# Kernel tuning notes

Hardware: AMD Instinct MI355X
Metric: run time of the kernel (lower is better)

## Reference

```python
import jax, jax.numpy as jnp
import numpy as np

B, N, D = 4, 4096, 256


def setup_inputs() -> dict:
    key = jax.random.key(0)
    k1, k2 = jax.random.split(key)
    val = jax.random.normal(k1, (B, N, D), dtype=jnp.float32)
    state = jax.random.normal(k2, (B, N), dtype=jnp.float32)
    return {"val": val, "state": state}


def reference(val, state):
    # pairwise_fn: scaled dot-product -> scores [B, N, N]
    scale = val.shape[-1] ** -0.5
    scores = jnp.einsum("bid,bjd->bij", val, val) * scale
    # edge_compress_fn = softsign (non-softmax compression)
    edges = scores / (1.0 + jnp.abs(scores))
    # state_weight_edges=False, val/state projections are Identity
    delta_state = jnp.einsum("bij,bj->bi", edges, state)   # [B, N]
    delta_val = jnp.einsum("bij,bjd->bid", edges, val)      # [B, N, D]
    return (delta_state, delta_val)
```

## Files before the change

kernel.cpp:

```cpp
#include <hip/hip_runtime.h>


#define B_  4
#define N_  4096
#define D_  256

typedef __attribute__((ext_vector_type(8))) short short8;
typedef __attribute__((ext_vector_type(4))) float floatx4;

__device__ __forceinline__ unsigned short f2bf(float f) {
    unsigned int u = __float_as_uint(f);
    u += 0x7fff + ((u >> 16) & 1);
    return (unsigned short)(u >> 16);
}

__device__ __forceinline__ void gl_lds16(const void* g, void* l) {
    __builtin_amdgcn_global_load_lds(
        (const __attribute__((address_space(1))) unsigned int*)g,
        (__attribute__((address_space(3))) unsigned int*)l, 16, 0, 0);
}
__device__ __forceinline__ void gl_lds4(const void* g, void* l) {
    __builtin_amdgcn_global_load_lds(
        (const __attribute__((address_space(1))) unsigned int*)g,
        (__attribute__((address_space(3))) unsigned int*)l, 4, 0, 0);
}

__global__ __launch_bounds__(256)
void prepass_kernel(const float* __restrict__ val,
                    unsigned short* __restrict__ Vb,
                    unsigned short* __restrict__ VF) {
    __shared__ unsigned short tile[64][68];
    const int t   = threadIdx.x;
    const int blk = blockIdx.x;
    const int b   = blk >> 8;
    const int it  = (blk >> 2) & 63;
    const int dt  = blk & 3;
    const int i0  = it * 64, d0 = dt * 64;
    const float*    vb  = val + (size_t)b * N_ * D_;
    unsigned short* Vbb = Vb  + (size_t)b * N_ * D_;
    unsigned short* VFb = VF  + (size_t)b * N_ * D_;

    #pragma unroll
    for (int q = 0; q < 4; ++q) {
        int idx = t + 256 * q;
        int row = idx >> 4;
        int c4  = idx & 15;
        float4 v = *(const float4*)(vb + (size_t)(i0 + row) * D_ + d0 + c4 * 4);
        ushort4 h;
        h.x = f2bf(v.x); h.y = f2bf(v.y); h.z = f2bf(v.z); h.w = f2bf(v.w);
        *(ushort4*)(Vbb + (size_t)(i0 + row) * D_ + d0 + c4 * 4) = h;
        *(ushort4*)&tile[row][c4 * 4] = h;
    }
    __syncthreads();
    #pragma unroll
    for (int q = 0; q < 4; ++q) {
        int dr = (t >> 4) + q * 16;
        int i4 = t & 15;
        ushort4 h;
        h.x = tile[i4 * 4 + 0][dr];
        h.y = tile[i4 * 4 + 1][dr];
        h.z = tile[i4 * 4 + 2][dr];
        h.w = tile[i4 * 4 + 3][dr];
        const int jb = (i0 >> 5) + (i4 >> 3);
        const int e  = (i4 & 7) * 4;
        *(ushort4*)(VFb + ((size_t)jb * 256 + d0 + dr) * 32 + e) = h;
    }
}

__global__ __launch_bounds__(256, 2)
void prop_main(const float* __restrict__ state,
               const unsigned short* __restrict__ Vb,
               const unsigned short* __restrict__ VF,
               float* __restrict__ dvp,
               float* __restrict__ dsp_o)
{
    __shared__ __attribute__((aligned(16))) unsigned char smem[75776];

    const int t    = threadIdx.x;
    const int w    = t >> 6;
    const int lane = t & 63;
    const int quad = lane >> 4;
    const int l16  = lane & 15;

    const int x   = blockIdx.x;
    const int it  = x >> 3;
    const int b   = (x >> 1) & 3;
    const int jh  = x & 1;
    const int it0 = it * 64;
    const int jbase = jh * 2048;
    const int niter = 32;

    unsigned short* EshL = (unsigned short*)(smem + 65536);
    float*          dsred = (float*)(smem + 75264);

    const unsigned short* Vbb = Vb + (size_t)b * N_ * D_;
    const unsigned short* VFb = VF + (size_t)b * N_ * D_;
    const float*          stb = state + (size_t)b * N_;

    const int hi  = lane >> 5;
    const int p32 = lane & 31;

    int vgoff[8];
    #pragma unroll
    for (int n = 0; n < 8; ++n) {
        int r  = 2 * (w * 8 + n) + hi;
        int gr = p32 ^ (r & 7);
        vgoff[n] = r * 256 + gr * 8;
    }

    const int r0 = (w >> 1) * 32;
    const int c0 = (w & 1) * 32;
    const int pA = l16 & 7;

    const unsigned short* vf_lane = VFb + (size_t)jh * (64 * 8192)
                                  + w * 2048 + l16 * 32 + quad * 8;

    short8 A0[8], A1[8];
    {
        const unsigned short* ar0 = Vbb + (size_t)(it0 + r0 + l16) * 256 + quad * 8;
        const unsigned short* ar1 = ar0 + 16 * 256;
        #pragma unroll
        for (int ks = 0; ks < 8; ++ks) {
            A0[ks] = *(const short8*)(ar0 + ks * 32);
            A1[ks] = *(const short8*)(ar1 + ks * 32);
        }
    }

    #pragma unroll
    for (int n = 0; n < 8; ++n)
        gl_lds16(Vbb + (size_t)jbase * 256 + vgoff[n],
                 smem + (w * 8 + n) * 1024);
    if (w == 0) gl_lds4(stb + jbase + lane, smem + 74752);

    floatx4 dv[4][4];
    #pragma unroll
    for (int a = 0; a < 4; ++a)
        #pragma unroll
        for (int c = 0; c < 4; ++c)
            dv[a][c] = (floatx4){0.f, 0.f, 0.f, 0.f};
    float dsp[8];
    #pragma unroll
    for (int k = 0; k < 8; ++k) dsp[k] = 0.f;

    for (int k = 0; k < niter; ++k) {
        const int buf = k & 1;
        unsigned short* vjL = (unsigned short*)(smem + buf * 32768);
        const float*    stj = (const float*)(smem + 74752 + buf * 256);

        __syncthreads();

        if (k + 1 < niter) {
            const size_t j0n = jbase + (size_t)(k + 1) * 64;
            #pragma unroll
            for (int n = 0; n < 8; ++n)
                gl_lds16(Vbb + j0n * 256 + vgoff[n],
                         smem + (buf ^ 1) * 32768 + (w * 8 + n) * 1024);
            if (w == 0) gl_lds4(stb + j0n + lane, smem + 74752 + (buf ^ 1) * 256);
        }

        short8 bfr[2][4];
        {
            const unsigned short* vfk = vf_lane + (size_t)k * 16384;
            #pragma unroll
            for (int ks = 0; ks < 2; ++ks)
                #pragma unroll
                for (int c2 = 0; c2 < 4; ++c2)
                    bfr[ks][c2] = *(const short8*)(vfk + ks * 8192 + c2 * 512);
        }

        floatx4 sa[2][2];
        #pragma unroll
        for (int a = 0; a < 2; ++a)
            #pragma unroll
            for (int c = 0; c < 2; ++c)
                sa[a][c] = (floatx4){0.f, 0.f, 0.f, 0.f};

        #pragma unroll
        for (int ks = 0; ks < 8; ++ks) {
            const int p = ((ks * 4 + quad) ^ pA) * 8;
            short8 b0 = *(const short8*)&vjL[(c0 + l16) * 256 + p];
            short8 b1 = *(const short8*)&vjL[(c0 + 16 + l16) * 256 + p];
            sa[0][0] = __builtin_amdgcn_mfma_f32_16x16x32_bf16(A0[ks], b0, sa[0][0], 0, 0, 0);
            sa[0][1] = __builtin_amdgcn_mfma_f32_16x16x32_bf16(A0[ks], b1, sa[0][1], 0, 0, 0);
            sa[1][0] = __builtin_amdgcn_mfma_f32_16x16x32_bf16(A1[ks], b0, sa[1][0], 0, 0, 0);
            sa[1][1] = __builtin_amdgcn_mfma_f32_16x16x32_bf16(A1[ks], b1, sa[1][1], 0, 0, 0);
        }

        float stc0 = stj[c0 + l16];
        float stc1 = stj[c0 + 16 + l16];
        #pragma unroll
        for (int a = 0; a < 2; ++a) {
            #pragma unroll
            for (int r = 0; r < 4; ++r) {
                const int il = r0 + a * 16 + quad * 4 + r;
                float s0 = sa[a][0][r];
                float s1 = sa[a][1][r];
                float e0 = s0 * __builtin_amdgcn_rcpf(16.0f + fabsf(s0));
                float e1 = s1 * __builtin_amdgcn_rcpf(16.0f + fabsf(s1));
                dsp[a * 4 + r] += e0 * stc0 + e1 * stc1;
                EshL[il * 72 + c0 + l16]      = f2bf(e0);
                EshL[il * 72 + c0 + 16 + l16] = f2bf(e1);
            }
        }
        __syncthreads();

        #pragma unroll
        for (int ks = 0; ks < 2; ++ks) {
            short8 af[4];
            #pragma unroll
            for (int a2 = 0; a2 < 4; ++a2)
                af[a2] = *(const short8*)&EshL[(a2 * 16 + l16) * 72 + ks * 32 + quad * 8];
            #pragma unroll
            for (int a2 = 0; a2 < 4; ++a2)
                #pragma unroll
                for (int c2 = 0; c2 < 4; ++c2)
                    dv[a2][c2] = __builtin_amdgcn_mfma_f32_16x16x32_bf16(af[a2], bfr[ks][c2], dv[a2][c2], 0, 0, 0);
        }
    }

    float* dvo = dvp + (size_t)jh * B_ * N_ * D_ + (size_t)b * N_ * D_
                     + (size_t)it0 * D_;
    #pragma unroll
    for (int a2 = 0; a2 < 4; ++a2)
        #pragma unroll
        for (int c2 = 0; c2 < 4; ++c2)
            #pragma unroll
            for (int r = 0; r < 4; ++r) {
                const int il = a2 * 16 + quad * 4 + r;
                const int d  = w * 64 + c2 * 16 + l16;
                dvo[(size_t)il * D_ + d] = dv[a2][c2][r];
            }

    #pragma unroll
    for (int k = 0; k < 8; ++k) {
        float v = dsp[k];
        v += __shfl_xor(v, 1);
        v += __shfl_xor(v, 2);
        v += __shfl_xor(v, 4);
        v += __shfl_xor(v, 8);
        dsp[k] = v;
    }
    if (l16 == 0) {
        #pragma unroll
        for (int a = 0; a < 2; ++a)
            #pragma unroll
            for (int r = 0; r < 4; ++r) {
                const int row = r0 + a * 16 + quad * 4 + r;
                dsred[(w & 1) * 64 + row] = dsp[a * 4 + r];
            }
    }
    __syncthreads();
    if (t < 64)
        dsp_o[(size_t)jh * B_ * N_ + (size_t)b * N_ + it0 + t]
            = dsred[t] + dsred[64 + t];
}

__global__ __launch_bounds__(256)
void combine_kernel(const float4* __restrict__ dv0, const float4* __restrict__ dv1,
                    const float*  __restrict__ ds0, const float*  __restrict__ ds1,
                    float* __restrict__ out) {
    const int NDV4 = B_ * N_ * D_ / 4;
    const int NDS  = B_ * N_;
    int x = blockIdx.x * 256 + threadIdx.x;
    if (x < NDV4) {
        float4 a = dv0[x], c = dv1[x];
        float4 r;
        r.x = a.x + c.x; r.y = a.y + c.y; r.z = a.z + c.z; r.w = a.w + c.w;
        ((float4*)(out + NDS))[x] = r;
    } else {
        int y = (x - NDV4) * 4;
        if (y < NDS) {
            float4 a = *(const float4*)(ds0 + y);
            float4 c = *(const float4*)(ds1 + y);
            float4 r;
            r.x = a.x + c.x; r.y = a.y + c.y; r.z = a.z + c.z; r.w = a.w + c.w;
            *(float4*)(out + y) = r;
        }
    }
}

__global__ __launch_bounds__(256, 1)
void prop_kernel_fb(const float* __restrict__ val,
                    const float* __restrict__ state,
                    float* __restrict__ out) {
    __shared__ __attribute__((aligned(16))) unsigned short vi[64][264];
    __shared__ __attribute__((aligned(16))) unsigned short vj[64][264];
    __shared__ __attribute__((aligned(16))) unsigned short vjt[2048][8];
    __shared__ __attribute__((aligned(16))) unsigned short Esh[64][72];
    __shared__ float stj[64];
    __shared__ float dsred[2][64];

    const int t    = threadIdx.x;
    const int w    = t >> 6;
    const int lane = t & 63;
    const int quad = lane >> 4;
    const int l16  = lane & 15;
    const int b   = blockIdx.x >> 6;
    const int it0 = (blockIdx.x & 63) << 6;
    const float* valb = val   + (size_t)b * N_ * D_;
    const float* stb  = state + (size_t)b * N_;

    #pragma unroll
    for (int n = 0; n < 16; ++n) {
        int idx = t + 256 * n;
        int row = idx >> 6;
        int c4  = idx & 63;
        float4 v = *(const float4*)(valb + (size_t)(it0 + row) * D_ + c4 * 4);
        ushort4 h;
        h.x = f2bf(v.x); h.y = f2bf(v.y); h.z = f2bf(v.z); h.w = f2bf(v.w);
        *(ushort4*)&vi[row][c4 * 4] = h;
    }

    const int r0 = (w >> 1) * 32;
    const int c0 = (w & 1) * 32;
    floatx4 dv[4][4];
    #pragma unroll
    for (int a = 0; a < 4; ++a)
        #pragma unroll
        for (int c = 0; c < 4; ++c)
            dv[a][c] = (floatx4){0.f, 0.f, 0.f, 0.f};
    float dsp[8];
    #pragma unroll
    for (int k = 0; k < 8; ++k) dsp[k] = 0.f;

    for (int jt = 0; jt < 64; ++jt) {
        const int j0 = jt * 64;
        #pragma unroll
        for (int n = 0; n < 16; ++n) {
            int idx = t + 256 * n;
            int row = idx >> 6;
            int c4  = idx & 63;
            float4 v = *(const float4*)(valb + (size_t)(j0 + row) * D_ + c4 * 4);
            ushort4 h;
            h.x = f2bf(v.x); h.y = f2bf(v.y); h.z = f2bf(v.z); h.w = f2bf(v.w);
            *(ushort4*)&vj[row][c4 * 4] = h;
        }
        if (t < 64) stj[t] = stb[j0 + t];
        __syncthreads();

        #pragma unroll
        for (int n = 0; n < 8; ++n) {
            const int d  = t;
            const int jb = n;
            short8 pk;
            #pragma unroll
            for (int jj = 0; jj < 8; ++jj) pk[jj] = (short)vj[jb * 8 + jj][d];
            *(short8*)&vjt[d * 8 + (jb ^ (d & 7))][0] = pk;
        }

        floatx4 sa[2][2];
        #pragma unroll
        for (int a = 0; a < 2; ++a)
            #pragma unroll
            for (int c = 0; c < 2; ++c)
                sa[a][c] = (floatx4){0.f, 0.f, 0.f, 0.f};
        #pragma unroll
        for (int ks = 0; ks < 8; ++ks) {
            const int d0 = ks * 32 + quad * 8;
            short8 a0 = *(const short8*)&vi[r0 + l16][d0];
            short8 a1 = *(const short8*)&vi[r0 + 16 + l16][d0];
            short8 b0 = *(const short8*)&vj[c0 + l16][d0];
            short8 b1 = *(const short8*)&vj[c0 + 16 + l16][d0];
            sa[0][0] = __builtin_amdgcn_mfma_f32_16x16x32_bf16(a0, b0, sa[0][0], 0, 0, 0);
            sa[0][1] = __builtin_amdgcn_mfma_f32_16x16x32_bf16(a0, b1, sa[0][1], 0, 0, 0);
            sa[1][0] = __builtin_amdgcn_mfma_f32_16x16x32_bf16(a1, b0, sa[1][0], 0, 0, 0);
            sa[1][1] = __builtin_amdgcn_mfma_f32_16x16x32_bf16(a1, b1, sa[1][1], 0, 0, 0);
        }

        float stc0 = stj[c0 + l16];
        float stc1 = stj[c0 + 16 + l16];
        #pragma unroll
        for (int a = 0; a < 2; ++a) {
            #pragma unroll
            for (int r = 0; r < 4; ++r) {
                const int il = r0 + a * 16 + quad * 4 + r;
                float s0 = sa[a][0][r] * 0.0625f;
                float s1 = sa[a][1][r] * 0.0625f;
                float e0 = s0 / (1.0f + fabsf(s0));
                float e1 = s1 / (1.0f + fabsf(s1));
                dsp[a * 4 + r] += e0 * stc0 + e1 * stc1;
                Esh[il][c0 + l16]      = f2bf(e0);
                Esh[il][c0 + 16 + l16] = f2bf(e1);
            }
        }
        __syncthreads();

        #pragma unroll
        for (int ks = 0; ks < 2; ++ks) {
            short8 af[4], bfr[4];
            #pragma unroll
            for (int a2 = 0; a2 < 4; ++a2)
                af[a2] = *(const short8*)&Esh[a2 * 16 + l16][ks * 32 + quad * 8];
            #pragma unroll
            for (int c2 = 0; c2 < 4; ++c2) {
                const int d  = w * 64 + c2 * 16 + l16;
                const int jb = ks * 4 + quad;
                bfr[c2] = *(const short8*)&vjt[d * 8 + (jb ^ (d & 7))][0];
            }
            #pragma unroll
            for (int a2 = 0; a2 < 4; ++a2)
                #pragma unroll
                for (int c2 = 0; c2 < 4; ++c2)
                    dv[a2][c2] = __builtin_amdgcn_mfma_f32_16x16x32_bf16(af[a2], bfr[c2], dv[a2][c2], 0, 0, 0);
        }
    }

    float* dvo = out + (size_t)B_ * N_ + (size_t)b * N_ * D_;
    #pragma unroll
    for (int a2 = 0; a2 < 4; ++a2)
        #pragma unroll
        for (int c2 = 0; c2 < 4; ++c2)
            #pragma unroll
            for (int r = 0; r < 4; ++r) {
                const int i = it0 + a2 * 16 + quad * 4 + r;
                const int d = w * 64 + c2 * 16 + l16;
                dvo[(size_t)i * D_ + d] = dv[a2][c2][r];
            }

    #pragma unroll
    for (int k = 0; k < 8; ++k) {
        float v = dsp[k];
        v += __shfl_xor(v, 1);
        v += __shfl_xor(v, 2);
        v += __shfl_xor(v, 4);
        v += __shfl_xor(v, 8);
        dsp[k] = v;
    }
    if (l16 == 0) {
        #pragma unroll
        for (int a = 0; a < 2; ++a)
            #pragma unroll
            for (int r = 0; r < 4; ++r) {
                const int row = (w >> 1) * 32 + a * 16 + quad * 4 + r;
                dsred[w & 1][row] = dsp[a * 4 + r];
            }
    }
    __syncthreads();
    if (t < 64) out[(size_t)b * N_ + it0 + t] = dsred[0][t] + dsred[1][t];
}

extern "C" void kernel_launch(void* const* d_in, const int* in_sizes, int n_in,
                              void* d_out, int out_size, void* d_ws, size_t ws_size,
                              hipStream_t stream) {
    const float* val   = (const float*)d_in[0];
    const float* state = (const float*)d_in[1];
    float* out = (float*)d_out;

    const size_t nE         = (size_t)B_ * N_ * D_;
    const size_t need_base  = 2 * nE * sizeof(unsigned short);
    const size_t need_split = need_base + 2 * nE * sizeof(float)
                            + 2 * (size_t)B_ * N_ * sizeof(float);

    if (ws_size >= need_split) {
        unsigned short* Vb = (unsigned short*)d_ws;
        unsigned short* VF = Vb + nE;
        float* dvp = (float*)(VF + nE);
        float* dsp = dvp + 2 * nE;
        prepass_kernel<<<dim3(1024), dim3(256), 0, stream>>>(val, Vb, VF);
        prop_main<<<dim3(512), dim3(256), 0, stream>>>(state, Vb, VF, dvp, dsp);
        const int NDV4 = B_ * N_ * D_ / 4;
        const int NDS4 = B_ * N_ / 4;
        combine_kernel<<<dim3((NDV4 + NDS4) / 256), dim3(256), 0, stream>>>(
            (const float4*)dvp, (const float4*)(dvp + nE),
            dsp, dsp + (size_t)B_ * N_, out);
    } else {
        prop_kernel_fb<<<dim3(256), dim3(256), 0, stream>>>(val, state, out);
    }
}
```

Baseline: 152.0 us.

## Load score-GEMM B operand directly from fragment-packed global layout, drop LDS staging

Result: slower. 244.9 us (+61.1%).

```diff
diff --git a/kernel.cpp b/kernel.cpp
--- a/kernel.cpp
+++ b/kernel.cpp
@@ -14,20 +14,9 @@
     return (unsigned short)(u >> 16);
 }
 
-__device__ __forceinline__ void gl_lds16(const void* g, void* l) {
-    __builtin_amdgcn_global_load_lds(
-        (const __attribute__((address_space(1))) unsigned int*)g,
-        (__attribute__((address_space(3))) unsigned int*)l, 16, 0, 0);
-}
-__device__ __forceinline__ void gl_lds4(const void* g, void* l) {
-    __builtin_amdgcn_global_load_lds(
-        (const __attribute__((address_space(1))) unsigned int*)g,
-        (__attribute__((address_space(3))) unsigned int*)l, 4, 0, 0);
-}
-
 __global__ __launch_bounds__(256)
 void prepass_kernel(const float* __restrict__ val,
-                    unsigned short* __restrict__ Vb,
+                    unsigned short* __restrict__ VG1,
                     unsigned short* __restrict__ VF) {
     __shared__ unsigned short tile[64][68];
     const int t   = threadIdx.x;
@@ -36,19 +25,23 @@
     const int it  = (blk >> 2) & 63;
     const int dt  = blk & 3;
     const int i0  = it * 64, d0 = dt * 64;
-    const float*    vb  = val + (size_t)b * N_ * D_;
-    unsigned short* Vbb = Vb  + (size_t)b * N_ * D_;
-    unsigned short* VFb = VF  + (size_t)b * N_ * D_;
+    const float*    vb   = val + (size_t)b * N_ * D_;
+    unsigned short* VG1b = VG1 + (size_t)b * N_ * D_;
+    unsigned short* VFb  = VF  + (size_t)b * N_ * D_;
 
     #pragma unroll
     for (int q = 0; q < 4; ++q) {
         int idx = t + 256 * q;
         int row = idx >> 4;
         int c4  = idx & 15;
-        float4 v = *(const float4*)(vb + (size_t)(i0 + row) * D_ + d0 + c4 * 4);
+        const int j = i0 + row;
+        const int d = d0 + c4 * 4;
+        float4 v = *(const float4*)(vb + (size_t)j * D_ + d);
         ushort4 h;
         h.x = f2bf(v.x); h.y = f2bf(v.y); h.z = f2bf(v.z); h.w = f2bf(v.w);
-        *(ushort4*)(Vbb + (size_t)(i0 + row) * D_ + d0 + c4 * 4) = h;
+        const size_t off = ((size_t)(j >> 4) * 8 + (d >> 5)) * 512
+                         + (j & 15) * 32 + (d & 31);
+        *(ushort4*)(VG1b + off) = h;
         *(ushort4*)&tile[row][c4 * 4] = h;
     }
     __syncthreads();
@@ -67,14 +60,14 @@
     }
 }
 
-__global__ __launch_bounds__(256, 2)
+__global__ __launch_bounds__(256, 3)
 void prop_main(const float* __restrict__ state,
-               const unsigned short* __restrict__ Vb,
+               const unsigned short* __restrict__ VG1,
                const unsigned short* __restrict__ VF,
                float* __restrict__ dvp,
                float* __restrict__ dsp_o)
 {
-    __shared__ __attribute__((aligned(16))) unsigned char smem[75776];
+    __shared__ __attribute__((aligned(16))) unsigned char smem[18944];
 
     const int t    = threadIdx.x;
     const int w    = t >> 6;
@@ -90,47 +83,31 @@
     const int jbase = jh * 2048;
     const int niter = 32;
 
-    unsigned short* EshL = (unsigned short*)(smem + 65536);
-    float*          dsred = (float*)(smem + 75264);
-
-    const unsigned short* Vbb = Vb + (size_t)b * N_ * D_;
-    const unsigned short* VFb = VF + (size_t)b * N_ * D_;
-    const float*          stb = state + (size_t)b * N_;
-
-    const int hi  = lane >> 5;
-    const int p32 = lane & 31;
-
-    int vgoff[8];
-    #pragma unroll
-    for (int n = 0; n < 8; ++n) {
-        int r  = 2 * (w * 8 + n) + hi;
-        int gr = p32 ^ (r & 7);
-        vgoff[n] = r * 256 + gr * 8;
-    }
+    float* dsred = (float*)(smem + 18432);
+
+    const unsigned short* VG1b = VG1 + (size_t)b * N_ * D_;
+    const unsigned short* VFb  = VF  + (size_t)b * N_ * D_;
+    const float*          stb  = state + (size_t)b * N_;
 
     const int r0 = (w >> 1) * 32;
     const int c0 = (w & 1) * 32;
-    const int pA = l16 & 7;
-
-    const unsigned short* vf_lane = VFb + (size_t)jh * (64 * 8192)
-                                  + w * 2048 + l16 * 32 + quad * 8;
 
     short8 A0[8], A1[8];
     {
-        const unsigned short* ar0 = Vbb + (size_t)(it0 + r0 + l16) * 256 + quad * 8;
-        const unsigned short* ar1 = ar0 + 16 * 256;
+        const unsigned short* a0p = VG1b + (size_t)((it0 + r0) >> 4) * 4096
+                                  + l16 * 32 + quad * 8;
         #pragma unroll
         for (int ks = 0; ks < 8; ++ks) {
-            A0[ks] = *(const short8*)(ar0 + ks * 32);
-            A1[ks] = *(const short8*)(ar1 + ks * 32);
-        }
-    }
-
-    #pragma unroll
-    for (int n = 0; n < 8; ++n)
-        gl_lds16(Vbb + (size_t)jbase * 256 + vgoff[n],
-                 smem + (w * 8 + n) * 1024);
-    if (w == 0) gl_lds4(stb + jbase + lane, smem + 74752);
+            A0[ks] = *(const short8*)(a0p + ks * 512);
+            A1[ks] = *(const short8*)(a0p + 4096 + ks * 512);
+        }
+    }
+
+    const unsigned short* g1p = VG1b + (size_t)((jbase + c0) >> 4) * 4096
+                              + l16 * 32 + quad * 8;
+
+    const unsigned short* vfp = VFb + (size_t)(jbase >> 5) * 8192
+                              + (w * 64 + l16) * 32 + quad * 8;
 
     floatx4 dv[4][4];
     #pragma unroll
@@ -144,23 +121,33 @@
 
     for (int k = 0; k < niter; ++k) {
         const int buf = k & 1;
-        unsigned short* vjL = (unsigned short*)(smem + buf * 32768);
-        const float*    stj = (const float*)(smem + 74752 + buf * 256);
-
-        __syncthreads();
-
-        if (k + 1 < niter) {
-            const size_t j0n = jbase + (size_t)(k + 1) * 64;
-            #pragma unroll
-            for (int n = 0; n < 8; ++n)
-                gl_lds16(Vbb + j0n * 256 + vgoff[n],
-                         smem + (buf ^ 1) * 32768 + (w * 8 + n) * 1024);
-            if (w == 0) gl_lds4(stb + j0n + lane, smem + 74752 + (buf ^ 1) * 256);
+        unsigned short* Eshg = (unsigned short*)(smem + buf * 9216);
+        const int j0 = jbase + k * 64;
+
+        float stc0 = stb[j0 + c0 + l16];
+        float stc1 = stb[j0 + c0 + 16 + l16];
+
+        floatx4 sa[2][2];
+        #pragma unroll
+        for (int a = 0; a < 2; ++a)
+            #pragma unroll
+            for (int c = 0; c < 2; ++c)
+                sa[a][c] = (floatx4){0.f, 0.f, 0.f, 0.f};
+
+        const unsigned short* g1k = g1p + (size_t)k * 16384;
+        #pragma unroll
+        for (int ks = 0; ks < 8; ++ks) {
+            short8 b0 = *(const short8*)(g1k + ks * 512);
+            short8 b1 = *(const short8*)(g1k + 4096 + ks * 512);
+            sa[0][0] = __builtin_amdgcn_mfma_f32_16x16x32_bf16(A0[ks], b0, sa[0][0], 0, 0, 0);
+            sa[0][1] = __builtin_amdgcn_mfma_f32_16x16x32_bf16(A0[ks], b1, sa[0][1], 0, 0, 0);
+            sa[1][0] = __builtin_amdgcn_mfma_f32_16x16x32_bf16(A1[ks], b0, sa[1][0], 0, 0, 0);
+            sa[1][1] = __builtin_amdgcn_mfma_f32_16x16x32_bf16(A1[ks], b1, sa[1][1], 0, 0, 0);
         }
 
         short8 bfr[2][4];
         {
-            const unsigned short* vfk = vf_lane + (size_t)k * 16384;
+            const unsigned short* vfk = vfp + (size_t)k * 16384;
             #pragma unroll
             for (int ks = 0; ks < 2; ++ks)
                 #pragma unroll
@@ -168,26 +155,6 @@
                     bfr[ks][c2] = *(const short8*)(vfk + ks * 8192 + c2 * 512);
         }
 
-        floatx4 sa[2][2];
-        #pragma unroll
-        for (int a = 0; a < 2; ++a)
-            #pragma unroll
-            for (int c = 0; c < 2; ++c)
-                sa[a][c] = (floatx4){0.f, 0.f, 0.f, 0.f};
-
-        #pragma unroll
-        for (int ks = 0; ks < 8; ++ks) {
-            const int p = ((ks * 4 + quad) ^ pA) * 8;
-            short8 b0 = *(const short8*)&vjL[(c0 + l16) * 256 + p];
-            short8 b1 = *(const short8*)&vjL[(c0 + 16 + l16) * 256 + p];
-            sa[0][0] = __builtin_amdgcn_mfma_f32_16x16x32_bf16(A0[ks], b0, sa[0][0], 0, 0, 0);
-            sa[0][1] = __builtin_amdgcn_mfma_f32_16x16x32_bf16(A0[ks], b1, sa[0][1], 0, 0, 0);
-            sa[1][0] = __builtin_amdgcn_mfma_f32_16x16x32_bf16(A1[ks], b0, sa[1][0], 0, 0, 0);
-            sa[1][1] = __builtin_amdgcn_mfma_f32_16x16x32_bf16(A1[ks], b1, sa[1][1], 0, 0, 0);
-        }
-
-        float stc0 = stj[c0 + l16];
-        float stc1 = stj[c0 + 16 + l16];
         #pragma unroll
         for (int a = 0; a < 2; ++a) {
             #pragma unroll
@@ -198,8 +165,8 @@
                 float e0 = s0 * __builtin_amdgcn_rcpf(16.0f + fabsf(s0));
                 float e1 = s1 * __builtin_amdgcn_rcpf(16.0f + fabsf(s1));
                 dsp[a * 4 + r] += e0 * stc0 + e1 * stc1;
-                EshL[il * 72 + c0 + l16]      = f2bf(e0);
-                EshL[il * 72 + c0 + 16 + l16] = f2bf(e1);
+                Eshg[il * 72 + c0 + l16]      = f2bf(e0);
+                Eshg[il * 72 + c0 + 16 + l16] = f2bf(e1);
             }
         }
         __syncthreads();
@@ -209,7 +176,7 @@
             short8 af[4];
             #pragma unroll
             for (int a2 = 0; a2 < 4; ++a2)
-                af[a2] = *(const short8*)&EshL[(a2 * 16 + l16) * 72 + ks * 32 + quad * 8];
+                af[a2] = *(const short8*)&Eshg[(a2 * 16 + l16) * 72 + ks * 32 + quad * 8];
             #pragma unroll
             for (int a2 = 0; a2 < 4; ++a2)
                 #pragma unroll
@@ -452,12 +419,12 @@
                             + 2 * (size_t)B_ * N_ * sizeof(float);
 
     if (ws_size >= need_split) {
-        unsigned short* Vb = (unsigned short*)d_ws;
-        unsigned short* VF = Vb + nE;
+        unsigned short* VG1 = (unsigned short*)d_ws;
+        unsigned short* VF  = VG1 + nE;
         float* dvp = (float*)(VF + nE);
         float* dsp = dvp + 2 * nE;
-        prepass_kernel<<<dim3(1024), dim3(256), 0, stream>>>(val, Vb, VF);
-        prop_main<<<dim3(512), dim3(256), 0, stream>>>(state, Vb, VF, dvp, dsp);
+        prepass_kernel<<<dim3(1024), dim3(256), 0, stream>>>(val, VG1, VF);
+        prop_main<<<dim3(512), dim3(256), 0, stream>>>(state, VG1, VF, dvp, dsp);
         const int NDV4 = B_ * N_ * D_ / 4;
         const int NDS4 = B_ * N_ / 4;
         combine_kernel<<<dim3((NDV4 + NDS4) / 256), dim3(256), 0, stream>>>(
```

## Replace split-K over j with 32-row i tiles and drop combine kernel

Applied to the files above, without the earlier changes.

Measured after the change: 170.9 us. 12.4% more time.

```diff
diff --git a/kernel.cpp b/kernel.cpp
--- a/kernel.cpp
+++ b/kernel.cpp
@@ -71,27 +71,25 @@
 void prop_main(const float* __restrict__ state,
                const unsigned short* __restrict__ Vb,
                const unsigned short* __restrict__ VF,
-               float* __restrict__ dvp,
-               float* __restrict__ dsp_o)
+               float* __restrict__ out)
 {
-    __shared__ __attribute__((aligned(16))) unsigned char smem[75776];
+    __shared__ __attribute__((aligned(16))) unsigned char smem[70656];
 
     const int t    = threadIdx.x;
     const int w    = t >> 6;
     const int lane = t & 63;
     const int quad = lane >> 4;
     const int l16  = lane & 15;
+    const int l7   = lane & 7;
 
     const int x   = blockIdx.x;
-    const int it  = x >> 3;
     const int b   = (x >> 1) & 3;
-    const int jh  = x & 1;
-    const int it0 = it * 64;
-    const int jbase = jh * 2048;
-    const int niter = 32;
-
-    unsigned short* EshL = (unsigned short*)(smem + 65536);
-    float*          dsred = (float*)(smem + 75264);
+    const int it  = ((x >> 3) << 1) | (x & 1);
+    const int it0 = it * 32;
+    const int niter = 64;
+
+    unsigned short* EshL  = (unsigned short*)(smem + 65536);
+    float*          dsred = (float*)(smem + 70144);
 
     const unsigned short* Vbb = Vb + (size_t)b * N_ * D_;
     const unsigned short* VFb = VF + (size_t)b * N_ * D_;
@@ -108,16 +106,15 @@
         vgoff[n] = r * 256 + gr * 8;
     }
 
-    const int r0 = (w >> 1) * 32;
-    const int c0 = (w & 1) * 32;
-    const int pA = l16 & 7;
-
-    const unsigned short* vf_lane = VFb + (size_t)jh * (64 * 8192)
-                                  + w * 2048 + l16 * 32 + quad * 8;
+    const int c0  = w * 16;
+    const int pA  = l7;
+    const int cbw = w * 2 + (l16 >> 3);
+
+    const unsigned short* vf_lane = VFb + (w * 64 + l16) * 32 + quad * 8;
 
     short8 A0[8], A1[8];
     {
-        const unsigned short* ar0 = Vbb + (size_t)(it0 + r0 + l16) * 256 + quad * 8;
+        const unsigned short* ar0 = Vbb + (size_t)(it0 + l16) * 256 + quad * 8;
         const unsigned short* ar1 = ar0 + 16 * 256;
         #pragma unroll
         for (int ks = 0; ks < 8; ++ks) {
@@ -128,13 +125,12 @@
 
     #pragma unroll
     for (int n = 0; n < 8; ++n)
-        gl_lds16(Vbb + (size_t)jbase * 256 + vgoff[n],
-                 smem + (w * 8 + n) * 1024);
-    if (w == 0) gl_lds4(stb + jbase + lane, smem + 74752);
-
-    floatx4 dv[4][4];
-    #pragma unroll
-    for (int a = 0; a < 4; ++a)
+        gl_lds16(Vbb + vgoff[n], smem + (w * 8 + n) * 1024);
+    if (w == 0) gl_lds4(stb + lane, smem + 69632);
+
+    floatx4 dv[2][4];
+    #pragma unroll
+    for (int a = 0; a < 2; ++a)
         #pragma unroll
         for (int c = 0; c < 4; ++c)
             dv[a][c] = (floatx4){0.f, 0.f, 0.f, 0.f};
@@ -145,17 +141,17 @@
     for (int k = 0; k < niter; ++k) {
         const int buf = k & 1;
         unsigned short* vjL = (unsigned short*)(smem + buf * 32768);
-        const float*    stj = (const float*)(smem + 74752 + buf * 256);
+        const float*    stj = (const float*)(smem + 69632 + buf * 256);
 
         __syncthreads();
 
         if (k + 1 < niter) {
-            const size_t j0n = jbase + (size_t)(k + 1) * 64;
+            const size_t j0n = (size_t)(k + 1) * 64;
             #pragma unroll
             for (int n = 0; n < 8; ++n)
                 gl_lds16(Vbb + j0n * 256 + vgoff[n],
                          smem + (buf ^ 1) * 32768 + (w * 8 + n) * 1024);
-            if (w == 0) gl_lds4(stb + j0n + lane, smem + 74752 + (buf ^ 1) * 256);
+            if (w == 0) gl_lds4(stb + j0n + lane, smem + 69632 + (buf ^ 1) * 256);
         }
 
         short8 bfr[2][4];
@@ -168,60 +164,52 @@
                     bfr[ks][c2] = *(const short8*)(vfk + ks * 8192 + c2 * 512);
         }
 
-        floatx4 sa[2][2];
-        #pragma unroll
-        for (int a = 0; a < 2; ++a)
-            #pragma unroll
-            for (int c = 0; c < 2; ++c)
-                sa[a][c] = (floatx4){0.f, 0.f, 0.f, 0.f};
-
+        floatx4 sa[2];
+        sa[0] = (floatx4){0.f, 0.f, 0.f, 0.f};
+        sa[1] = (floatx4){0.f, 0.f, 0.f, 0.f};
         #pragma unroll
         for (int ks = 0; ks < 8; ++ks) {
             const int p = ((ks * 4 + quad) ^ pA) * 8;
-            short8 b0 = *(const short8*)&vjL[(c0 + l16) * 256 + p];
-            short8 b1 = *(const short8*)&vjL[(c0 + 16 + l16) * 256 + p];
-            sa[0][0] = __builtin_amdgcn_mfma_f32_16x16x32_bf16(A0[ks], b0, sa[0][0], 0, 0, 0);
-            sa[0][1] = __builtin_amdgcn_mfma_f32_16x16x32_bf16(A0[ks], b1, sa[0][1], 0, 0, 0);
-            sa[1][0] = __builtin_amdgcn_mfma_f32_16x16x32_bf16(A1[ks], b0, sa[1][0], 0, 0, 0);
-            sa[1][1] = __builtin_amdgcn_mfma_f32_16x16x32_bf16(A1[ks], b1, sa[1][1], 0, 0, 0);
-        }
-
-        float stc0 = stj[c0 + l16];
-        float stc1 = stj[c0 + 16 + l16];
+            short8 bb = *(const short8*)&vjL[(c0 + l16) * 256 + p];
+            sa[0] = __builtin_amdgcn_mfma_f32_16x16x32_bf16(A0[ks], bb, sa[0], 0, 0, 0);
+            sa[1] = __builtin_amdgcn_mfma_f32_16x16x32_bf16(A1[ks], bb, sa[1], 0, 0, 0);
+        }
+
+        float stc = stj[c0 + l16];
         #pragma unroll
         for (int a = 0; a < 2; ++a) {
             #pragma unroll
             for (int r = 0; r < 4; ++r) {
-                const int il = r0 + a * 16 + quad * 4 + r;
-                float s0 = sa[a][0][r];
-                float s1 = sa[a][1][r];
-                float e0 = s0 * __builtin_amdgcn_rcpf(16.0f + fabsf(s0));
-                float e1 = s1 * __builtin_amdgcn_rcpf(16.0f + fabsf(s1));
-                dsp[a * 4 + r] += e0 * stc0 + e1 * stc1;
-                EshL[il * 72 + c0 + l16]      = f2bf(e0);
-                EshL[il * 72 + c0 + 16 + l16] = f2bf(e1);
+                const int il  = a * 16 + quad * 4 + r;
+                const int key = (il & 7) ^ ((il >> 3) << 1);
+                float s = sa[a][r];
+                float e = s * __builtin_amdgcn_rcpf(16.0f + fabsf(s));
+                dsp[a * 4 + r] += e * stc;
+                EshL[il * 64 + ((cbw ^ key) << 3) + l7] = f2bf(e);
             }
         }
         __syncthreads();
 
         #pragma unroll
         for (int ks = 0; ks < 2; ++ks) {
-            short8 af[4];
-            #pragma unroll
-            for (int a2 = 0; a2 < 4; ++a2)
-                af[a2] = *(const short8*)&EshL[(a2 * 16 + l16) * 72 + ks * 32 + quad * 8];
-            #pragma unroll
-            for (int a2 = 0; a2 < 4; ++a2)
+            short8 af[2];
+            #pragma unroll
+            for (int a2 = 0; a2 < 2; ++a2) {
+                const int keyr = l7 ^ ((a2 * 2 + (l16 >> 3)) << 1);
+                af[a2] = *(const short8*)&EshL[(a2 * 16 + l16) * 64
+                                               + (((ks * 4 + quad) ^ keyr) << 3)];
+            }
+            #pragma unroll
+            for (int a2 = 0; a2 < 2; ++a2)
                 #pragma unroll
                 for (int c2 = 0; c2 < 4; ++c2)
                     dv[a2][c2] = __builtin_amdgcn_mfma_f32_16x16x32_bf16(af[a2], bfr[ks][c2], dv[a2][c2], 0, 0, 0);
         }
     }
 
-    float* dvo = dvp + (size_t)jh * B_ * N_ * D_ + (size_t)b * N_ * D_
-                     + (size_t)it0 * D_;
-    #pragma unroll
-    for (int a2 = 0; a2 < 4; ++a2)
+    float* dvo = out + (size_t)B_ * N_ + (size_t)b * N_ * D_ + (size_t)it0 * D_;
+    #pragma unroll
+    for (int a2 = 0; a2 < 2; ++a2)
         #pragma unroll
         for (int c2 = 0; c2 < 4; ++c2)
             #pragma unroll
@@ -245,38 +233,14 @@
         for (int a = 0; a < 2; ++a)
             #pragma unroll
             for (int r = 0; r < 4; ++r) {
-                const int row = r0 + a * 16 + quad * 4 + r;
-                dsred[(w & 1) * 64 + row] = dsp[a * 4 + r];
+                const int row = a * 16 + quad * 4 + r;
+                dsred[w * 32 + row] = dsp[a * 4 + r];
             }
     }
     __syncthreads();
-    if (t < 64)
-        dsp_o[(size_t)jh * B_ * N_ + (size_t)b * N_ + it0 + t]
-            = dsred[t] + dsred[64 + t];
-}
-
-__global__ __launch_bounds__(256)
-void combine_kernel(const float4* __restrict__ dv0, const float4* __restrict__ dv1,
-                    const float*  __restrict__ ds0, const float*  __restrict__ ds1,
-                    float* __restrict__ out) {
-    const int NDV4 = B_ * N_ * D_ / 4;
-    const int NDS  = B_ * N_;
-    int x = blockIdx.x * 256 + threadIdx.x;
-    if (x < NDV4) {
-        float4 a = dv0[x], c = dv1[x];
-        float4 r;
-        r.x = a.x + c.x; r.y = a.y + c.y; r.z = a.z + c.z; r.w = a.w + c.w;
-        ((float4*)(out + NDS))[x] = r;
-    } else {
-        int y = (x - NDV4) * 4;
-        if (y < NDS) {
-            float4 a = *(const float4*)(ds0 + y);
-            float4 c = *(const float4*)(ds1 + y);
-            float4 r;
-            r.x = a.x + c.x; r.y = a.y + c.y; r.z = a.z + c.z; r.w = a.w + c.w;
-            *(float4*)(out + y) = r;
-        }
-    }
+    if (t < 32)
+        out[(size_t)b * N_ + it0 + t]
+            = dsred[t] + dsred[32 + t] + dsred[64 + t] + dsred[96 + t];
 }
 
 __global__ __launch_bounds__(256, 1)
@@ -446,23 +410,14 @@
     const float* state = (const float*)d_in[1];
     float* out = (float*)d_out;
 
-    const size_t nE         = (size_t)B_ * N_ * D_;
-    const size_t need_base  = 2 * nE * sizeof(unsigned short);
-    const size_t need_split = need_base + 2 * nE * sizeof(float)
-                            + 2 * (size_t)B_ * N_ * sizeof(float);
-
-    if (ws_size >= need_split) {
+    const size_t nE        = (size_t)B_ * N_ * D_;
+    const size_t need_base = 2 * nE * sizeof(unsigned short);
+
+    if (ws_size >= need_base) {
         unsigned short* Vb = (unsigned short*)d_ws;
         unsigned short* VF = Vb + nE;
-        float* dvp = (float*)(VF + nE);
-        float* dsp = dvp + 2 * nE;
         prepass_kernel<<<dim3(1024), dim3(256), 0, stream>>>(val, Vb, VF);
-        prop_main<<<dim3(512), dim3(256), 0, stream>>>(state, Vb, VF, dvp, dsp);
-        const int NDV4 = B_ * N_ * D_ / 4;
-        const int NDS4 = B_ * N_ / 4;
-        combine_kernel<<<dim3((NDV4 + NDS4) / 256), dim3(256), 0, stream>>>(
-            (const float4*)dvp, (const float4*)(dvp + nE),
-            dsp, dsp + (size_t)B_ * N_, out);
+        prop_main<<<dim3(512), dim3(256), 0, stream>>>(state, Vb, VF, out);
     } else {
         prop_kernel_fb<<<dim3(256), dim3(256), 0, stream>>>(val, state, out);
     }
```
